# Kernel tuning notes

Hardware: AMD Instinct MI355X
Metric: run time of the kernel (lower is better)

## Reference

```python
import jax, jax.numpy as jnp
import numpy as np

B, M, K, F, H = 4096, 50000, 31, 256, 256
N = K + 1                      # nodes per graph: center + K neighbors
GAMMA = 1.0 / (2.0 * 1.0 ** 2) # rbf_kernel gamma with length_scale = 1.0


def setup_inputs() -> dict:
    key = jax.random.key(0)
    k = jax.random.split(key, 9)
    return {
        "spatial_features": jax.random.normal(k[0], (B, 2), jnp.float32),
        "features": jax.random.normal(k[1], (B, F), jnp.float32),
        "train_spatial": jax.random.normal(k[2], (M, 2), jnp.float32),
        "train_features": jax.random.normal(k[3], (M, F), jnp.float32),
        "train_y": jax.random.normal(k[4], (M, 1), jnp.float32),
        "W0": jax.random.normal(k[5], (F + 2, H), jnp.float32) * (1.0 / np.sqrt(F + 2)),
        "W1": jax.random.normal(k[6], (H, H), jnp.float32) * (1.0 / np.sqrt(H)),
        "W2": jax.random.normal(k[7], (H, H), jnp.float32) * (1.0 / np.sqrt(H)),
        "Wout": jax.random.normal(k[8], (H, 1), jnp.float32) * (1.0 / np.sqrt(H)),
    }


def reference(spatial_features, features, train_spatial, train_features, train_y,
              W0, W1, W2, Wout):
    # --- brute-force kNN over train spatial coords (sklearn kneighbors) ---
    d2 = (jnp.sum(spatial_features ** 2, -1, keepdims=True)
          - 2.0 * spatial_features @ train_spatial.T
          + jnp.sum(train_spatial ** 2, -1)[None, :])                 # [B, M]
    nb = jax.lax.top_k(jax.lax.stop_gradient(-d2), K)[1]              # [B, K] indices

    # --- form_input_graph: node features = [feat ++ y ++ indicator] ---
    feat = jnp.concatenate([features[:, None, :], train_features[nb]], axis=1)    # [B,N,F]
    y = jnp.concatenate([jnp.zeros((B, 1, 1), feat.dtype), train_y[nb]], axis=1)  # [B,N,1]
    ind = jnp.zeros((B, N, 1), feat.dtype).at[:, 0, 0].set(1.0)                   # [B,N,1]
    x = jnp.concatenate([feat, y, ind], axis=-1)                                  # [B,N,F+2]

    # --- dense RBF adjacency: complete graph, self-loops already on diagonal ---
    coords = jnp.concatenate([spatial_features[:, None, :], train_spatial[nb]], axis=1)  # [B,N,2]
    diff = coords[:, :, None, :] - coords[:, None, :, :]
    A = jnp.exp(-GAMMA * jnp.sum(diff * diff, -1))                    # [B,N,N]
    # GCN symmetric normalization D^-1/2 A D^-1/2 (deg > 0 since diag = 1)
    dinv = jax.lax.rsqrt(jnp.sum(A, -1))                              # [B,N]
    Ahat = A * dinv[:, :, None] * dinv[:, None, :]

    h = jax.nn.relu(jnp.einsum('bij,bjh->bih', Ahat, x @ W0))
    h = jax.nn.relu(jnp.einsum('bij,bjh->bih', Ahat, h @ W1))
    h = jax.nn.relu(jnp.einsum('bij,bjh->bih', Ahat, h @ W2))

    # center node -> linear head (bias=False), last_activation='none'
    return h[:, 0] @ Wout                                             # [B, 1]
```

## Files before the change

### kernel.cpp

```cpp
#include <hip/hip_runtime.h>

typedef _Float16 half8 __attribute__((ext_vector_type(8)));
typedef __fp16  fp16x2 __attribute__((ext_vector_type(2)));
typedef float f32x16 __attribute__((ext_vector_type(16)));

#define M_TRAIN 50000
#define NQ 4096
#define KNN 31

#define LO_SCALE 1024.0f
#define LO_INV   9.765625e-4f

__global__ void prep_weights_k(const float* __restrict__ W0,
                               const float* __restrict__ W1,
                               const float* __restrict__ W2,
                               _Float16* __restrict__ W0hi, _Float16* __restrict__ W0lo,
                               _Float16* __restrict__ W1hi, _Float16* __restrict__ W1lo,
                               _Float16* __restrict__ W2hi, _Float16* __restrict__ W2lo) {
    int t = blockIdx.x * 256 + threadIdx.x;
    const int n0 = 17 * 8 * 64, n1 = 16 * 8 * 64, n2 = 16 * 8 * 64;
    if (t >= n0 + n1 + n2) return;
    const float* src; _Float16 *dhi, *dlo; int idx, Kin;
    if (t < n0)           { src = W0; dhi = W0hi; dlo = W0lo; idx = t;           Kin = 258; }
    else if (t < n0 + n1) { src = W1; dhi = W1hi; dlo = W1lo; idx = t - n0;      Kin = 256; }
    else                  { src = W2; dhi = W2hi; dlo = W2lo; idx = t - n0 - n1; Kin = 256; }
    int lane = idx & 63, nt = (idx >> 6) & 7, ks = idx >> 9;
    int col = nt * 32 + (lane & 31);
    int k0  = ks * 16 + (lane >> 5) * 8;
    _Float16 vhi[8], vlo[8];
#pragma unroll
    for (int j = 0; j < 8; j++) {
        int k = k0 + j;
        float w = (k < Kin) ? src[k * 256 + col] : 0.f;
        _Float16 hi = (_Float16)w;
        vhi[j] = hi;
        vlo[j] = (_Float16)((w - (float)hi) * LO_SCALE);
    }
    *reinterpret_cast<uint4*>(dhi + (size_t)idx * 8) = *reinterpret_cast<const uint4*>(vhi);
    *reinterpret_cast<uint4*>(dlo + (size_t)idx * 8) = *reinterpret_cast<const uint4*>(vlo);
}

#define QPB2 4
#define TILE2 2048
#define CAP2 128

__global__ __launch_bounds__(256) void knn_k(const float* __restrict__ qs,
                                             const float* __restrict__ ts,
                                             int* __restrict__ nb) {
    __shared__ __align__(16) float tile[TILE2 * 2];
    __shared__ float  mrg[QPB2][128];
    __shared__ int    ci[QPB2][CAP2];
    __shared__ double chd[QPB2][CAP2];
    __shared__ int    cnt[QPB2];

    const int t = threadIdx.x;
    const int w = t >> 6, lane = t & 63;
    const int q = blockIdx.x * QPB2 + w;

    if (lane == 0) cnt[w] = 0;
    const float qx = qs[q * 2 + 0], qy = qs[q * 2 + 1];
    const float2* tilev = reinterpret_cast<const float2*>(tile);

    float v0 = 3.4e38f, v1 = 3.4e38f;
    for (int base = 0; base < M_TRAIN; base += TILE2) {
        const int n = min(TILE2, M_TRAIN - base);
        __syncthreads();
        for (int i = t; i < n / 2; i += 256)
            reinterpret_cast<float4*>(tile)[i] =
                reinterpret_cast<const float4*>(ts + (size_t)base * 2)[i];
        __syncthreads();
#pragma unroll 4
        for (int p = lane; p < n; p += 64) {
            float2 pt = tilev[p];
            float dx = qx - pt.x, dy = qy - pt.y;
            float d2 = fmaf(dx, dx, dy * dy);
            v1 = fminf(v1, fmaxf(v0, d2));
            v0 = fminf(v0, d2);
        }
    }
    __syncthreads();
    mrg[w][2 * lane]     = v0;
    mrg[w][2 * lane + 1] = v1;
    __syncthreads();

    float xa = mrg[w][lane], xb = mrg[w][64 + lane];
    int lea = 0, leb = 0;
    for (int i = 0; i < 128; i++) {
        float v = mrg[w][i];
        lea += (v <= xa) ? 1 : 0;
        leb += (v <= xb) ? 1 : 0;
    }
    float tc = 3.4e38f;
    if (lea >= 31) tc = xa;
    if (leb >= 31 && xb < tc) tc = xb;
#pragma unroll
    for (int off = 32; off; off >>= 1)
        tc = fminf(tc, __shfl_xor(tc, off));
    const float thr = tc * 1.00001f + 1e-7f;

    for (int base = 0; base < M_TRAIN; base += TILE2) {
        const int n = min(TILE2, M_TRAIN - base);
        __syncthreads();
        for (int i = t; i < n / 2; i += 256)
            reinterpret_cast<float4*>(tile)[i] =
                reinterpret_cast<const float4*>(ts + (size_t)base * 2)[i];
        __syncthreads();
#pragma unroll 4
        for (int p = lane; p < n; p += 64) {
            float2 pt = tilev[p];
            float dx = qx - pt.x, dy = qy - pt.y;
            float d2 = fmaf(dx, dx, dy * dy);
            if (d2 < thr) {
                int pos = atomicAdd(&cnt[w], 1);
                if (pos < CAP2) ci[w][pos] = base + p;
            }
        }
    }
    __syncthreads();

    const int C = min(cnt[w], CAP2);
    for (int c = lane; c < C; c += 64) {
        int idx = ci[w][c];
        double dx = (double)qx - (double)ts[idx * 2];
        double dy = (double)qy - (double)ts[idx * 2 + 1];
        chd[w][c] = dx * dx + dy * dy;
    }
    __syncthreads();
    for (int c = lane; c < C; c += 64) {
        double key = chd[w][c];
        int   idx = ci[w][c];
        int rank = 0;
        for (int o = 0; o < C; o++) {
            double ok = chd[w][o];
            int    oi = ci[w][o];
            rank += ((ok < key) || (ok == key && oi < idx)) ? 1 : 0;
        }
        if (rank < KNN) nb[q * KNN + rank] = idx;
    }
}

#define PX 276
#define PT 36

__device__ inline half8 ld_h8(const _Float16* p) {
    union { half8 h; uint2 u[2]; } r;
    r.u[0] = *reinterpret_cast<const uint2*>(p);
    r.u[1] = *reinterpret_cast<const uint2*>(p + 4);
    return r.h;
}
__device__ inline half8 ld_h8_g(const _Float16* p) {
    union { half8 h; uint4 u; } r;
    r.u = *reinterpret_cast<const uint4*>(p);
    return r.h;
}
__device__ inline f32x16 zero16() {
    f32x16 z;
#pragma unroll
    for (int i = 0; i < 16; i++) z[i] = 0.f;
    return z;
}
__device__ inline unsigned pk_u(float a, float b) {
    union { fp16x2 v; unsigned u; } c;
    c.v = __builtin_amdgcn_cvt_pkrtz(a, b);
    return c.u;
}
__device__ inline float f16lo(unsigned u) {
    union { unsigned u; fp16x2 v; } c; c.u = u; return (float)c.v[0];
}
__device__ inline float f16hi(unsigned u) {
    union { unsigned u; fp16x2 v; } c; c.u = u; return (float)c.v[1];
}
__device__ inline half8 frag_x(const unsigned* w, int ks2, int h) {
    unsigned w0 = w[4 * ks2 + 0], w1 = w[4 * ks2 + 1];
    unsigned w2 = w[4 * ks2 + 2], w3 = w[4 * ks2 + 3];
    unsigned sA = h ? w0 : w2, sB = h ? w1 : w3;
    unsigned rA = __shfl_xor(sA, 32);
    unsigned rB = __shfl_xor(sB, 32);
    unsigned kA = h ? w2 : w0, kB = h ? w3 : w1;
    union { half8 h8; unsigned u[4]; } f;
    f.u[0] = h ? rA : kA;
    f.u[1] = h ? rB : kB;
    f.u[2] = h ? kA : rA;
    f.u[3] = h ? kB : rB;
    return f.h8;
}
#define MFMA(a, b, c) __builtin_amdgcn_mfma_f32_32x32x16_f16((a), (b), (c), 0, 0, 0)

__global__ __launch_bounds__(256, 4) void gcn_k(
    const float* __restrict__ qs, const float* __restrict__ qf,
    const float* __restrict__ ts, const float* __restrict__ tf,
    const float* __restrict__ ty, const float* __restrict__ Wout,
    const int* __restrict__ nb,
    const _Float16* __restrict__ W0hi, const _Float16* __restrict__ W0lo,
    const _Float16* __restrict__ W1hi, const _Float16* __restrict__ W1lo,
    const _Float16* __restrict__ W2hi, const _Float16* __restrict__ W2lo,
    float* __restrict__ out) {
    __shared__ __align__(16) _Float16 Xhi[32 * PX];
    __shared__ __align__(16) _Float16 Xlo[32 * PX];
    __shared__ _Float16 Ahhi[32 * PT];
    __shared__ _Float16 Ahlo[32 * PT];
    __shared__ float coords[64];
    __shared__ float dinv[32];
    __shared__ float yvs[32];
    __shared__ int   idxs[32];

    const int t = threadIdx.x;
    const int w = t >> 6, lane = t & 63;
    const int h = lane >> 5, ln = lane & 31;
    const int q0 = blockIdx.x;

    if (t < 32) {
        int idx = (t == 0) ? -1 : nb[q0 * KNN + (t - 1)];
        idxs[t] = idx;
        const float* c = (t == 0) ? (qs + (size_t)q0 * 2) : (ts + (size_t)idx * 2);
        coords[t * 2 + 0] = c[0];
        coords[t * 2 + 1] = c[1];
        yvs[t] = (t == 0) ? 0.f : ty[idx];
    }
    __syncthreads();

    {
        const float* src0 = (w == 0) ? (qf + (size_t)q0 * 256)
                                     : (tf + (size_t)idxs[w] * 256);
        float4 pv = reinterpret_cast<const float4*>(src0)[lane];
        for (int r = w; r < 32; r += 4) {
            float4 cv = pv;
            int rn = r + 4;
            if (rn < 32)
                pv = reinterpret_cast<const float4*>(tf + (size_t)idxs[rn] * 256)[lane];
            float a4[4] = {cv.x, cv.y, cv.z, cv.w};
            unsigned hw[2], lw[2];
#pragma unroll
            for (int j = 0; j < 2; j++) {
                float x0 = a4[2 * j], x1 = a4[2 * j + 1];
                hw[j] = pk_u(x0, x1);
                lw[j] = pk_u((x0 - f16lo(hw[j])) * LO_SCALE,
                             (x1 - f16hi(hw[j])) * LO_SCALE);
            }
            *reinterpret_cast<uint2*>(&Xhi[r * PX + 4 * lane]) = *reinterpret_cast<uint2*>(hw);
            *reinterpret_cast<uint2*>(&Xlo[r * PX + 4 * lane]) = *reinterpret_cast<uint2*>(lw);
            if (lane == 0) {
                float yv = yvs[r];
                _Float16 thi[16], tlo[16];
#pragma unroll
                for (int j = 0; j < 16; j++) { thi[j] = (_Float16)0.f; tlo[j] = (_Float16)0.f; }
                _Float16 yh = (_Float16)yv;
                thi[0] = yh;
                tlo[0] = (_Float16)((yv - (float)yh) * LO_SCALE);
                thi[1] = (r == 0) ? (_Float16)1.f : (_Float16)0.f;
#pragma unroll
                for (int c = 0; c < 4; c++) {
                    *reinterpret_cast<uint2*>(&Xhi[r * PX + 256 + 4 * c]) = reinterpret_cast<uint2*>(thi)[c];
                    *reinterpret_cast<uint2*>(&Xlo[r * PX + 256 + 4 * c]) = reinterpret_cast<uint2*>(tlo)[c];
                }
            }
        }
    }

    if (t < 64) {
        int i = t >> 1, jh = t & 1;
        float xi = coords[i * 2], yi = coords[i * 2 + 1];
        float part = 0.f;
#pragma unroll
        for (int jj = 0; jj < 16; jj++) {
            int j = jh * 16 + jj;
            float dx = xi - coords[j * 2], dy = yi - coords[j * 2 + 1];
            part += __expf(-0.5f * (dx * dx + dy * dy));
        }
        float asum = part + __shfl_xor(part, 1);
        if (jh == 0) dinv[i] = 1.0f / sqrtf(asum);
    }
    __syncthreads();
    if (t < 64) {
        int i = t >> 1, jh = t & 1;
        float xi = coords[i * 2], yi = coords[i * 2 + 1];
        float di = dinv[i];
        _Float16 ahi[16], alo[16];
#pragma unroll
        for (int jj = 0; jj < 16; jj++) {
            int j = jh * 16 + jj;
            float dx = xi - coords[j * 2], dy = yi - coords[j * 2 + 1];
            float a = __expf(-0.5f * (dx * dx + dy * dy)) * di * dinv[j];
            _Float16 hi = (_Float16)a;
            ahi[jj] = hi;
            alo[jj] = (_Float16)((a - (float)hi) * LO_SCALE);
        }
        _Float16* dh = &Ahhi[i * PT + jh * 16];
        _Float16* dl = &Ahlo[i * PT + jh * 16];
#pragma unroll
        for (int c = 0; c < 4; c++) {
            reinterpret_cast<uint2*>(dh)[c] = reinterpret_cast<uint2*>(ahi)[c];
            reinterpret_cast<uint2*>(dl)[c] = reinterpret_cast<uint2*>(alo)[c];
        }
    }
    __syncthreads();

    const _Float16* Whis[3] = {W0hi, W1hi, W2hi};
    const _Float16* Wlos[3] = {W0lo, W1lo, W2lo};
    for (int layer = 0; layer < 3; layer++) {
        const _Float16* Whi = Whis[layer];
        const _Float16* Wlo = Wlos[layer];
        const int KS = (layer == 0) ? 17 : 16;

        f32x16 acc0 = zero16(), acc1 = zero16();
        f32x16 cor0 = zero16(), cor1 = zero16();
        const int boBase = (2 * w * 64 + lane) * 8;
        const _Float16* Xa = &Xhi[ln * PX + 8 * h];
        const _Float16* Xb = &Xlo[ln * PX + 8 * h];
#pragma unroll 2
        for (int ks = 0; ks < KS; ks++) {
            half8 Ahi_ = ld_h8(Xa + ks * 16);
            half8 Alo_ = ld_h8(Xb + ks * 16);
            int bo = boBase + ks * 4096;
            half8 Bh0 = ld_h8_g(Whi + bo);
            half8 Bh1 = ld_h8_g(Whi + bo + 512);
            half8 Bl0 = ld_h8_g(Wlo + bo);
            half8 Bl1 = ld_h8_g(Wlo + bo + 512);
            acc0 = MFMA(Ahi_, Bh0, acc0);
            cor0 = MFMA(Alo_, Bh0, cor0);
            cor0 = MFMA(Ahi_, Bl0, cor0);
            acc1 = MFMA(Ahi_, Bh1, acc1);
            cor1 = MFMA(Alo_, Bh1, cor1);
            cor1 = MFMA(Ahi_, Bl1, cor1);
        }
        __syncthreads();

        unsigned whi0[8], wlo0[8], whi1[8], wlo1[8];
#pragma unroll
        for (int g = 0; g < 8; g++) {
            float x0 = fmaf(cor0[2 * g],     LO_INV, acc0[2 * g]);
            float x1 = fmaf(cor0[2 * g + 1], LO_INV, acc0[2 * g + 1]);
            unsigned hw = pk_u(x0, x1);
            whi0[g] = hw;
            wlo0[g] = pk_u((x0 - f16lo(hw)) * LO_SCALE, (x1 - f16hi(hw)) * LO_SCALE);
            float y0 = fmaf(cor1[2 * g],     LO_INV, acc1[2 * g]);
            float y1 = fmaf(cor1[2 * g + 1], LO_INV, acc1[2 * g + 1]);
            unsigned hv = pk_u(y0, y1);
            whi1[g] = hv;
            wlo1[g] = pk_u((y0 - f16lo(hv)) * LO_SCALE, (y1 - f16hi(hv)) * LO_SCALE);
        }

        f32x16 p0 = zero16(), p1 = zero16();
        f32x16 pc0 = zero16(), pc1 = zero16();
#pragma unroll
        for (int ks2 = 0; ks2 < 2; ks2++) {
            half8 bAhi = ld_h8(&Ahhi[ln * PT + ks2 * 16 + 8 * h]);
            half8 bAlo = ld_h8(&Ahlo[ln * PT + ks2 * 16 + 8 * h]);
            half8 t0hi = frag_x(whi0, ks2, h);
            half8 t0lo = frag_x(wlo0, ks2, h);
            half8 t1hi = frag_x(whi1, ks2, h);
            half8 t1lo = frag_x(wlo1, ks2, h);
            p0  = MFMA(t0hi, bAhi, p0);
            pc0 = MFMA(t0lo, bAhi, pc0);
            pc0 = MFMA(t0hi, bAlo, pc0);
            p1  = MFMA(t1hi, bAhi, p1);
            pc1 = MFMA(t1lo, bAhi, pc1);
            pc1 = MFMA(t1hi, bAlo, pc1);
        }

#pragma unroll
        for (int a = 0; a < 2; a++) {
            const f32x16& A = a ? p1 : p0;
            const f32x16& C = a ? pc1 : pc0;
#pragma unroll
            for (int c = 0; c < 4; c++) {
                float x0 = fmaf(C[4 * c + 0], LO_INV, A[4 * c + 0]);
                float x1 = fmaf(C[4 * c + 1], LO_INV, A[4 * c + 1]);
                float x2 = fmaf(C[4 * c + 2], LO_INV, A[4 * c + 2]);
                float x3 = fmaf(C[4 * c + 3], LO_INV, A[4 * c + 3]);
                x0 = fmaxf(x0, 0.f); x1 = fmaxf(x1, 0.f);
                x2 = fmaxf(x2, 0.f); x3 = fmaxf(x3, 0.f);
                unsigned hw[2], lw[2];
                hw[0] = pk_u(x0, x1);
                hw[1] = pk_u(x2, x3);
                lw[0] = pk_u((x0 - f16lo(hw[0])) * LO_SCALE, (x1 - f16hi(hw[0])) * LO_SCALE);
                lw[1] = pk_u((x2 - f16lo(hw[1])) * LO_SCALE, (x3 - f16hi(hw[1])) * LO_SCALE);
                int feat = 64 * w + 32 * a + 8 * c + 4 * h;
                *reinterpret_cast<uint2*>(&Xhi[ln * PX + feat]) = *reinterpret_cast<uint2*>(hw);
                *reinterpret_cast<uint2*>(&Xlo[ln * PX + feat]) = *reinterpret_cast<uint2*>(lw);
            }
        }
        __syncthreads();
    }

    if (w == 0) {
        float4 wv = reinterpret_cast<const float4*>(Wout)[lane];
        union { uint2 u; _Float16 f[4]; } hh, hl;
        hh.u = *reinterpret_cast<const uint2*>(&Xhi[4 * lane]);
        hl.u = *reinterpret_cast<const uint2*>(&Xlo[4 * lane]);
        float s = ((float)hh.f[0] + (float)hl.f[0] * LO_INV) * wv.x
                + ((float)hh.f[1] + (float)hl.f[1] * LO_INV) * wv.y
                + ((float)hh.f[2] + (float)hl.f[2] * LO_INV) * wv.z
                + ((float)hh.f[3] + (float)hl.f[3] * LO_INV) * wv.w;
#pragma unroll
        for (int off = 32; off; off >>= 1) s += __shfl_xor(s, off);
        if (lane == 0) out[q0] = s;
    }
}

extern "C" void kernel_launch(void* const* d_in, const int* in_sizes, int n_in,
                              void* d_out, int out_size, void* d_ws, size_t ws_size,
                              hipStream_t stream) {
    const float* qs   = (const float*)d_in[0];
    const float* qf   = (const float*)d_in[1];
    const float* ts   = (const float*)d_in[2];
    const float* tf   = (const float*)d_in[3];
    const float* ty   = (const float*)d_in[4];
    const float* W0   = (const float*)d_in[5];
    const float* W1   = (const float*)d_in[6];
    const float* W2   = (const float*)d_in[7];
    const float* Wout = (const float*)d_in[8];
    float* out = (float*)d_out;

    char* ws = (char*)d_ws;
    int*      nb   = (int*)ws;
    _Float16* W0hi = (_Float16*)(ws + 524288);
    _Float16* W0lo = (_Float16*)(ws + 663552);
    _Float16* W1hi = (_Float16*)(ws + 802816);
    _Float16* W1lo = (_Float16*)(ws + 933888);
    _Float16* W2hi = (_Float16*)(ws + 1064960);
    _Float16* W2lo = (_Float16*)(ws + 1196032);

    hipLaunchKernelGGL(prep_weights_k, dim3(98), dim3(256), 0, stream,
                       W0, W1, W2, W0hi, W0lo, W1hi, W1lo, W2hi, W2lo);
    hipLaunchKernelGGL(knn_k, dim3(NQ / QPB2), dim3(256), 0, stream, qs, ts, nb);
    hipLaunchKernelGGL(gcn_k, dim3(NQ), dim3(256), 0, stream,
                       qs, qf, ts, tf, ty, Wout, nb,
                       W0hi, W0lo, W1hi, W1lo, W2hi, W2lo, out);
}
```

Measured before the change: 327.9 us.

## Process two queries per wave in kNN and split GCN across eight waves

The kNN kernel now gives each wave two queries. Every train point read from the shared tile is reused for two distance computations, and the tile size and queries per block are doubled. The GCN kernel moves to 512-thread blocks, where each wave owns 32 output columns instead of 64. This halves per-wave accumulator registers and MFMA chains, but needs more LDS per block in kNN and may reduce resident blocks.

Measured after the change: 366.6 us. +11.8%, slower.

```diff
diff --git a/kernel.cpp b/kernel.cpp
--- a/kernel.cpp
+++ b/kernel.cpp
@@ -40,8 +40,8 @@
     *reinterpret_cast<uint4*>(dlo + (size_t)idx * 8) = *reinterpret_cast<const uint4*>(vlo);
 }
 
-#define QPB2 4
-#define TILE2 2048
+#define QPB2 8
+#define TILE2 4096
 #define CAP2 128
 
 __global__ __launch_bounds__(256) void knn_k(const float* __restrict__ qs,
@@ -55,13 +55,15 @@
 
     const int t = threadIdx.x;
     const int w = t >> 6, lane = t & 63;
-    const int q = blockIdx.x * QPB2 + w;
-
-    if (lane == 0) cnt[w] = 0;
-    const float qx = qs[q * 2 + 0], qy = qs[q * 2 + 1];
+    const int q0 = blockIdx.x * QPB2;
+    const int qA = q0 + 2 * w, qB = qA + 1;
+
+    if (lane < 2) cnt[2 * w + lane] = 0;
+    const float qxA = qs[qA * 2 + 0], qyA = qs[qA * 2 + 1];
+    const float qxB = qs[qB * 2 + 0], qyB = qs[qB * 2 + 1];
     const float2* tilev = reinterpret_cast<const float2*>(tile);
 
-    float v0 = 3.4e38f, v1 = 3.4e38f;
+    float a0 = 3.4e38f, a1 = 3.4e38f, b0 = 3.4e38f, b1 = 3.4e38f;
     for (int base = 0; base < M_TRAIN; base += TILE2) {
         const int n = min(TILE2, M_TRAIN - base);
         __syncthreads();
@@ -72,31 +74,41 @@
 #pragma unroll 4
         for (int p = lane; p < n; p += 64) {
             float2 pt = tilev[p];
-            float dx = qx - pt.x, dy = qy - pt.y;
-            float d2 = fmaf(dx, dx, dy * dy);
-            v1 = fminf(v1, fmaxf(v0, d2));
-            v0 = fminf(v0, d2);
-        }
-    }
-    __syncthreads();
-    mrg[w][2 * lane]     = v0;
-    mrg[w][2 * lane + 1] = v1;
-    __syncthreads();
-
-    float xa = mrg[w][lane], xb = mrg[w][64 + lane];
-    int lea = 0, leb = 0;
-    for (int i = 0; i < 128; i++) {
-        float v = mrg[w][i];
-        lea += (v <= xa) ? 1 : 0;
-        leb += (v <= xb) ? 1 : 0;
-    }
-    float tc = 3.4e38f;
-    if (lea >= 31) tc = xa;
-    if (leb >= 31 && xb < tc) tc = xb;
-#pragma unroll
-    for (int off = 32; off; off >>= 1)
-        tc = fminf(tc, __shfl_xor(tc, off));
-    const float thr = tc * 1.00001f + 1e-7f;
+            float dxA = qxA - pt.x, dyA = qyA - pt.y;
+            float dA = fmaf(dxA, dxA, dyA * dyA);
+            a1 = fminf(a1, fmaxf(a0, dA));
+            a0 = fminf(a0, dA);
+            float dxB = qxB - pt.x, dyB = qyB - pt.y;
+            float dB = fmaf(dxB, dxB, dyB * dyB);
+            b1 = fminf(b1, fmaxf(b0, dB));
+            b0 = fminf(b0, dB);
+        }
+    }
+    __syncthreads();
+    mrg[2 * w + 0][2 * lane] = a0; mrg[2 * w + 0][2 * lane + 1] = a1;
+    mrg[2 * w + 1][2 * lane] = b0; mrg[2 * w + 1][2 * lane + 1] = b1;
+    __syncthreads();
+
+    float thrq[2];
+#pragma unroll
+    for (int qq = 0; qq < 2; qq++) {
+        const int qi = 2 * w + qq;
+        float xa = mrg[qi][lane], xb = mrg[qi][64 + lane];
+        int lea = 0, leb = 0;
+        for (int i = 0; i < 128; i++) {
+            float v = mrg[qi][i];
+            lea += (v <= xa) ? 1 : 0;
+            leb += (v <= xb) ? 1 : 0;
+        }
+        float tc = 3.4e38f;
+        if (lea >= 31) tc = xa;
+        if (leb >= 31 && xb < tc) tc = xb;
+#pragma unroll
+        for (int off = 32; off; off >>= 1)
+            tc = fminf(tc, __shfl_xor(tc, off));
+        thrq[qq] = tc * 1.00001f + 1e-7f;
+    }
+    const float thrA = thrq[0], thrB = thrq[1];
 
     for (int base = 0; base < M_TRAIN; base += TILE2) {
         const int n = min(TILE2, M_TRAIN - base);
@@ -108,34 +120,46 @@
 #pragma unroll 4
         for (int p = lane; p < n; p += 64) {
             float2 pt = tilev[p];
-            float dx = qx - pt.x, dy = qy - pt.y;
-            float d2 = fmaf(dx, dx, dy * dy);
-            if (d2 < thr) {
-                int pos = atomicAdd(&cnt[w], 1);
-                if (pos < CAP2) ci[w][pos] = base + p;
+            float dxA = qxA - pt.x, dyA = qyA - pt.y;
+            float dA = fmaf(dxA, dxA, dyA * dyA);
+            if (dA < thrA) {
+                int pos = atomicAdd(&cnt[2 * w + 0], 1);
+                if (pos < CAP2) ci[2 * w + 0][pos] = base + p;
             }
-        }
-    }
-    __syncthreads();
-
-    const int C = min(cnt[w], CAP2);
-    for (int c = lane; c < C; c += 64) {
-        int idx = ci[w][c];
-        double dx = (double)qx - (double)ts[idx * 2];
-        double dy = (double)qy - (double)ts[idx * 2 + 1];
-        chd[w][c] = dx * dx + dy * dy;
-    }
-    __syncthreads();
-    for (int c = lane; c < C; c += 64) {
-        double key = chd[w][c];
-        int   idx = ci[w][c];
-        int rank = 0;
-        for (int o = 0; o < C; o++) {
-            double ok = chd[w][o];
-            int    oi = ci[w][o];
-            rank += ((ok < key) || (ok == key && oi < idx)) ? 1 : 0;
-        }
-        if (rank < KNN) nb[q * KNN + rank] = idx;
+            float dxB = qxB - pt.x, dyB = qyB - pt.y;
+            float dB = fmaf(dxB, dxB, dyB * dyB);
+            if (dB < thrB) {
+                int pos = atomicAdd(&cnt[2 * w + 1], 1);
+                if (pos < CAP2) ci[2 * w + 1][pos] = base + p;
+            }
+        }
+    }
+    __syncthreads();
+
+#pragma unroll
+    for (int qq = 0; qq < 2; qq++) {
+        const int qi = 2 * w + qq;
+        const int q  = q0 + qi;
+        const float qx = qq ? qxB : qxA, qy = qq ? qyB : qyA;
+        const int C = min(cnt[qi], CAP2);
+        for (int c = lane; c < C; c += 64) {
+            int idx = ci[qi][c];
+            double dx = (double)qx - (double)ts[idx * 2];
+            double dy = (double)qy - (double)ts[idx * 2 + 1];
+            chd[qi][c] = dx * dx + dy * dy;
+        }
+        __syncthreads();
+        for (int c = lane; c < C; c += 64) {
+            double key = chd[qi][c];
+            int   idx = ci[qi][c];
+            int rank = 0;
+            for (int o = 0; o < C; o++) {
+                double ok = chd[qi][o];
+                int    oi = ci[qi][o];
+                rank += ((ok < key) || (ok == key && oi < idx)) ? 1 : 0;
+            }
+            if (rank < KNN) nb[q * KNN + rank] = idx;
+        }
     }
 }
 
@@ -186,7 +210,7 @@
 }
 #define MFMA(a, b, c) __builtin_amdgcn_mfma_f32_32x32x16_f16((a), (b), (c), 0, 0, 0)
 
-__global__ __launch_bounds__(256, 4) void gcn_k(
+__global__ __launch_bounds__(512, 8) void gcn_k(
     const float* __restrict__ qs, const float* __restrict__ qf,
     const float* __restrict__ ts, const float* __restrict__ tf,
     const float* __restrict__ ty, const float* __restrict__ Wout,
@@ -223,9 +247,9 @@
         const float* src0 = (w == 0) ? (qf + (size_t)q0 * 256)
                                      : (tf + (size_t)idxs[w] * 256);
         float4 pv = reinterpret_cast<const float4*>(src0)[lane];
-        for (int r = w; r < 32; r += 4) {
+        for (int r = w; r < 32; r += 8) {
             float4 cv = pv;
-            int rn = r + 4;
+            int rn = r + 8;
             if (rn < 32)
                 pv = reinterpret_cast<const float4*>(tf + (size_t)idxs[rn] * 256)[lane];
             float a4[4] = {cv.x, cv.y, cv.z, cv.w};
@@ -302,9 +326,9 @@
         const _Float16* Wlo = Wlos[layer];
         const int KS = (layer == 0) ? 17 : 16;
 
-        f32x16 acc0 = zero16(), acc1 = zero16();
-        f32x16 cor0 = zero16(), cor1 = zero16();
-        const int boBase = (2 * w * 64 + lane) * 8;
+        f32x16 acc = zero16();
+        f32x16 cor = zero16();
+        const int boBase = (w * 64 + lane) * 8;
         const _Float16* Xa = &Xhi[ln * PX + 8 * h];
         const _Float16* Xb = &Xlo[ln * PX + 8 * h];
 #pragma unroll 2
@@ -312,73 +336,52 @@
             half8 Ahi_ = ld_h8(Xa + ks * 16);
             half8 Alo_ = ld_h8(Xb + ks * 16);
             int bo = boBase + ks * 4096;
-            half8 Bh0 = ld_h8_g(Whi + bo);
-            half8 Bh1 = ld_h8_g(Whi + bo + 512);
-            half8 Bl0 = ld_h8_g(Wlo + bo);
-            half8 Bl1 = ld_h8_g(Wlo + bo + 512);
-            acc0 = MFMA(Ahi_, Bh0, acc0);
-            cor0 = MFMA(Alo_, Bh0, cor0);
-            cor0 = MFMA(Ahi_, Bl0, cor0);
-            acc1 = MFMA(Ahi_, Bh1, acc1);
-            cor1 = MFMA(Alo_, Bh1, cor1);
-            cor1 = MFMA(Ahi_, Bl1, cor1);
-        }
-        __syncthreads();
-
-        unsigned whi0[8], wlo0[8], whi1[8], wlo1[8];
+            half8 Bh = ld_h8_g(Whi + bo);
+            half8 Bl = ld_h8_g(Wlo + bo);
+            acc = MFMA(Ahi_, Bh, acc);
+            cor = MFMA(Alo_, Bh, cor);
+            cor = MFMA(Ahi_, Bl, cor);
+        }
+        __syncthreads();
+
+        unsigned whi[8], wlo[8];
 #pragma unroll
         for (int g = 0; g < 8; g++) {
-            float x0 = fmaf(cor0[2 * g],     LO_INV, acc0[2 * g]);
-            float x1 = fmaf(cor0[2 * g + 1], LO_INV, acc0[2 * g + 1]);
+            float x0 = fmaf(cor[2 * g],     LO_INV, acc[2 * g]);
+            float x1 = fmaf(cor[2 * g + 1], LO_INV, acc[2 * g + 1]);
             unsigned hw = pk_u(x0, x1);
-            whi0[g] = hw;
-            wlo0[g] = pk_u((x0 - f16lo(hw)) * LO_SCALE, (x1 - f16hi(hw)) * LO_SCALE);
-            float y0 = fmaf(cor1[2 * g],     LO_INV, acc1[2 * g]);
-            float y1 = fmaf(cor1[2 * g + 1], LO_INV, acc1[2 * g + 1]);
-            unsigned hv = pk_u(y0, y1);
-            whi1[g] = hv;
-            wlo1[g] = pk_u((y0 - f16lo(hv)) * LO_SCALE, (y1 - f16hi(hv)) * LO_SCALE);
-        }
-
-        f32x16 p0 = zero16(), p1 = zero16();
-        f32x16 pc0 = zero16(), pc1 = zero16();
+            whi[g] = hw;
+            wlo[g] = pk_u((x0 - f16lo(hw)) * LO_SCALE, (x1 - f16hi(hw)) * LO_SCALE);
+        }
+
+        f32x16 p = zero16(), pc = zero16();
 #pragma unroll
         for (int ks2 = 0; ks2 < 2; ks2++) {
             half8 bAhi = ld_h8(&Ahhi[ln * PT + ks2 * 16 + 8 * h]);
             half8 bAlo = ld_h8(&Ahlo[ln * PT + ks2 * 16 + 8 * h]);
-            half8 t0hi = frag_x(whi0, ks2, h);
-            half8 t0lo = frag_x(wlo0, ks2, h);
-            half8 t1hi = frag_x(whi1, ks2, h);
-            half8 t1lo = frag_x(wlo1, ks2, h);
-            p0  = MFMA(t0hi, bAhi, p0);
-            pc0 = MFMA(t0lo, bAhi, pc0);
-            pc0 = MFMA(t0hi, bAlo, pc0);
-            p1  = MFMA(t1hi, bAhi, p1);
-            pc1 = MFMA(t1lo, bAhi, pc1);
-            pc1 = MFMA(t1hi, bAlo, pc1);
-        }
-
-#pragma unroll
-        for (int a = 0; a < 2; a++) {
-            const f32x16& A = a ? p1 : p0;
-            const f32x16& C = a ? pc1 : pc0;
-#pragma unroll
-            for (int c = 0; c < 4; c++) {
-                float x0 = fmaf(C[4 * c + 0], LO_INV, A[4 * c + 0]);
-                float x1 = fmaf(C[4 * c + 1], LO_INV, A[4 * c + 1]);
-                float x2 = fmaf(C[4 * c + 2], LO_INV, A[4 * c + 2]);
-                float x3 = fmaf(C[4 * c + 3], LO_INV, A[4 * c + 3]);
-                x0 = fmaxf(x0, 0.f); x1 = fmaxf(x1, 0.f);
-                x2 = fmaxf(x2, 0.f); x3 = fmaxf(x3, 0.f);
-                unsigned hw[2], lw[2];
-                hw[0] = pk_u(x0, x1);
-                hw[1] = pk_u(x2, x3);
-                lw[0] = pk_u((x0 - f16lo(hw[0])) * LO_SCALE, (x1 - f16hi(hw[0])) * LO_SCALE);
-                lw[1] = pk_u((x2 - f16lo(hw[1])) * LO_SCALE, (x3 - f16hi(hw[1])) * LO_SCALE);
-                int feat = 64 * w + 32 * a + 8 * c + 4 * h;
-                *reinterpret_cast<uint2*>(&Xhi[ln * PX + feat]) = *reinterpret_cast<uint2*>(hw);
-                *reinterpret_cast<uint2*>(&Xlo[ln * PX + feat]) = *reinterpret_cast<uint2*>(lw);
-            }
+            half8 thi = frag_x(whi, ks2, h);
+            half8 tlo = frag_x(wlo, ks2, h);
+            p  = MFMA(thi, bAhi, p);
+            pc = MFMA(tlo, bAhi, pc);
+            pc = MFMA(thi, bAlo, pc);
+        }
+
+#pragma unroll
+        for (int c = 0; c < 4; c++) {
+            float x0 = fmaf(pc[4 * c + 0], LO_INV, p[4 * c + 0]);
+            float x1 = fmaf(pc[4 * c + 1], LO_INV, p[4 * c + 1]);
+            float x2 = fmaf(pc[4 * c + 2], LO_INV, p[4 * c + 2]);
+            float x3 = fmaf(pc[4 * c + 3], LO_INV, p[4 * c + 3]);
+            x0 = fmaxf(x0, 0.f); x1 = fmaxf(x1, 0.f);
+            x2 = fmaxf(x2, 0.f); x3 = fmaxf(x3, 0.f);
+            unsigned hw[2], lw[2];
+            hw[0] = pk_u(x0, x1);
+            hw[1] = pk_u(x2, x3);
+            lw[0] = pk_u((x0 - f16lo(hw[0])) * LO_SCALE, (x1 - f16hi(hw[0])) * LO_SCALE);
+            lw[1] = pk_u((x2 - f16lo(hw[1])) * LO_SCALE, (x3 - f16hi(hw[1])) * LO_SCALE);
+            int feat = 32 * w + 8 * c + 4 * h;
+            *reinterpret_cast<uint2*>(&Xhi[ln * PX + feat]) = *reinterpret_cast<uint2*>(hw);
+            *reinterpret_cast<uint2*>(&Xlo[ln * PX + feat]) = *reinterpret_cast<uint2*>(lw);
         }
         __syncthreads();
     }
@@ -424,7 +427,7 @@
     hipLaunchKernelGGL(prep_weights_k, dim3(98), dim3(256), 0, stream,
                        W0, W1, W2, W0hi, W0lo, W1hi, W1lo, W2hi, W2lo);
     hipLaunchKernelGGL(knn_k, dim3(NQ / QPB2), dim3(256), 0, stream, qs, ts, nb);
-    hipLaunchKernelGGL(gcn_k, dim3(NQ), dim3(256), 0, stream,
+    hipLaunchKernelGGL(gcn_k, dim3(NQ), dim3(512), 0, stream,
                        qs, qf, ts, tf, ty, Wout, nb,
                        W0hi, W0lo, W1hi, W1lo, W2hi, W2lo, out);
 }
```

## Process two query graphs per block to share weight fragment loads

Applied to the files above, without the earlier changes.

Each gcn block now handles two query graphs with 512 threads instead of one graph with 256 threads. Each of the eight waves covers 32 output features and reuses the same W hi/lo fragment for both graphs' 32-row tiles. This halves global weight traffic per graph and doubles the per-block LDS footprint. The risk is lower occupancy from the larger LDS and thread count, and a launch bound of 512x4 that may pressure registers.

Result: faster. 315.9 us, median of 2 (-3.7%).

```diff
diff --git a/kernel.cpp b/kernel.cpp
--- a/kernel.cpp
+++ b/kernel.cpp
@@ -186,7 +186,7 @@
 }
 #define MFMA(a, b, c) __builtin_amdgcn_mfma_f32_32x32x16_f16((a), (b), (c), 0, 0, 0)
 
-__global__ __launch_bounds__(256, 4) void gcn_k(
+__global__ __launch_bounds__(512, 4) void gcn_k(
     const float* __restrict__ qs, const float* __restrict__ qf,
     const float* __restrict__ ts, const float* __restrict__ tf,
     const float* __restrict__ ty, const float* __restrict__ Wout,
@@ -195,39 +195,43 @@
     const _Float16* __restrict__ W1hi, const _Float16* __restrict__ W1lo,
     const _Float16* __restrict__ W2hi, const _Float16* __restrict__ W2lo,
     float* __restrict__ out) {
-    __shared__ __align__(16) _Float16 Xhi[32 * PX];
-    __shared__ __align__(16) _Float16 Xlo[32 * PX];
-    __shared__ _Float16 Ahhi[32 * PT];
-    __shared__ _Float16 Ahlo[32 * PT];
-    __shared__ float coords[64];
-    __shared__ float dinv[32];
-    __shared__ float yvs[32];
-    __shared__ int   idxs[32];
+    __shared__ __align__(16) _Float16 Xhi[64 * PX];
+    __shared__ __align__(16) _Float16 Xlo[64 * PX];
+    __shared__ _Float16 Ahhi[2 * 32 * PT];
+    __shared__ _Float16 Ahlo[2 * 32 * PT];
+    __shared__ float coords[128];
+    __shared__ float dinv[64];
+    __shared__ float yvs[64];
+    __shared__ int   idxs[64];
 
     const int t = threadIdx.x;
     const int w = t >> 6, lane = t & 63;
     const int h = lane >> 5, ln = lane & 31;
-    const int q0 = blockIdx.x;
-
-    if (t < 32) {
-        int idx = (t == 0) ? -1 : nb[q0 * KNN + (t - 1)];
+    const int g2 = blockIdx.x * 2;
+
+    if (t < 64) {
+        int g = t >> 5, n = t & 31;
+        int idx = (n == 0) ? -1 : nb[(g2 + g) * KNN + (n - 1)];
         idxs[t] = idx;
-        const float* c = (t == 0) ? (qs + (size_t)q0 * 2) : (ts + (size_t)idx * 2);
+        const float* c = (n == 0) ? (qs + (size_t)(g2 + g) * 2) : (ts + (size_t)idx * 2);
         coords[t * 2 + 0] = c[0];
         coords[t * 2 + 1] = c[1];
-        yvs[t] = (t == 0) ? 0.f : ty[idx];
+        yvs[t] = (n == 0) ? 0.f : ty[idx];
     }
     __syncthreads();
 
     {
-        const float* src0 = (w == 0) ? (qf + (size_t)q0 * 256)
-                                     : (tf + (size_t)idxs[w] * 256);
-        float4 pv = reinterpret_cast<const float4*>(src0)[lane];
-        for (int r = w; r < 32; r += 4) {
+        const float* s0 = ((w & 31) == 0) ? (qf + (size_t)(g2 + (w >> 5)) * 256)
+                                          : (tf + (size_t)idxs[w] * 256);
+        float4 pv = reinterpret_cast<const float4*>(s0)[lane];
+        for (int r = w; r < 64; r += 8) {
             float4 cv = pv;
-            int rn = r + 4;
-            if (rn < 32)
-                pv = reinterpret_cast<const float4*>(tf + (size_t)idxs[rn] * 256)[lane];
+            int rn = r + 8;
+            if (rn < 64) {
+                const float* sn = ((rn & 31) == 0) ? (qf + (size_t)(g2 + (rn >> 5)) * 256)
+                                                   : (tf + (size_t)idxs[rn] * 256);
+                pv = reinterpret_cast<const float4*>(sn)[lane];
+            }
             float a4[4] = {cv.x, cv.y, cv.z, cv.w};
             unsigned hw[2], lw[2];
 #pragma unroll
@@ -247,7 +251,7 @@
                 _Float16 yh = (_Float16)yv;
                 thi[0] = yh;
                 tlo[0] = (_Float16)((yv - (float)yh) * LO_SCALE);
-                thi[1] = (r == 0) ? (_Float16)1.f : (_Float16)0.f;
+                thi[1] = ((r & 31) == 0) ? (_Float16)1.f : (_Float16)0.f;
 #pragma unroll
                 for (int c = 0; c < 4; c++) {
                     *reinterpret_cast<uint2*>(&Xhi[r * PX + 256 + 4 * c]) = reinterpret_cast<uint2*>(thi)[c];
@@ -257,36 +261,38 @@
         }
     }
 
-    if (t < 64) {
-        int i = t >> 1, jh = t & 1;
-        float xi = coords[i * 2], yi = coords[i * 2 + 1];
+    if (t < 128) {
+        int g = t >> 6, i = (t >> 1) & 31, jh = t & 1;
+        int ni = g * 32 + i;
+        float xi = coords[ni * 2], yi = coords[ni * 2 + 1];
         float part = 0.f;
 #pragma unroll
         for (int jj = 0; jj < 16; jj++) {
-            int j = jh * 16 + jj;
-            float dx = xi - coords[j * 2], dy = yi - coords[j * 2 + 1];
+            int nj = g * 32 + jh * 16 + jj;
+            float dx = xi - coords[nj * 2], dy = yi - coords[nj * 2 + 1];
             part += __expf(-0.5f * (dx * dx + dy * dy));
         }
         float asum = part + __shfl_xor(part, 1);
-        if (jh == 0) dinv[i] = 1.0f / sqrtf(asum);
-    }
-    __syncthreads();
-    if (t < 64) {
-        int i = t >> 1, jh = t & 1;
-        float xi = coords[i * 2], yi = coords[i * 2 + 1];
-        float di = dinv[i];
+        if (jh == 0) dinv[ni] = 1.0f / sqrtf(asum);
+    }
+    __syncthreads();
+    if (t < 128) {
+        int g = t >> 6, i = (t >> 1) & 31, jh = t & 1;
+        int ni = g * 32 + i;
+        float xi = coords[ni * 2], yi = coords[ni * 2 + 1];
+        float di = dinv[ni];
         _Float16 ahi[16], alo[16];
 #pragma unroll
         for (int jj = 0; jj < 16; jj++) {
-            int j = jh * 16 + jj;
-            float dx = xi - coords[j * 2], dy = yi - coords[j * 2 + 1];
-            float a = __expf(-0.5f * (dx * dx + dy * dy)) * di * dinv[j];
+            int nj = g * 32 + jh * 16 + jj;
+            float dx = xi - coords[nj * 2], dy = yi - coords[nj * 2 + 1];
+            float a = __expf(-0.5f * (dx * dx + dy * dy)) * di * dinv[nj];
             _Float16 hi = (_Float16)a;
             ahi[jj] = hi;
             alo[jj] = (_Float16)((a - (float)hi) * LO_SCALE);
         }
-        _Float16* dh = &Ahhi[i * PT + jh * 16];
-        _Float16* dl = &Ahlo[i * PT + jh * 16];
+        _Float16* dh = &Ahhi[ni * PT + jh * 16];
+        _Float16* dl = &Ahlo[ni * PT + jh * 16];
 #pragma unroll
         for (int c = 0; c < 4; c++) {
             reinterpret_cast<uint2*>(dh)[c] = reinterpret_cast<uint2*>(ahi)[c];
@@ -302,26 +308,28 @@
         const _Float16* Wlo = Wlos[layer];
         const int KS = (layer == 0) ? 17 : 16;
 
-        f32x16 acc0 = zero16(), acc1 = zero16();
-        f32x16 cor0 = zero16(), cor1 = zero16();
-        const int boBase = (2 * w * 64 + lane) * 8;
-        const _Float16* Xa = &Xhi[ln * PX + 8 * h];
-        const _Float16* Xb = &Xlo[ln * PX + 8 * h];
+        f32x16 acc0 = zero16(), cor0 = zero16();
+        f32x16 acc1 = zero16(), cor1 = zero16();
+        const int boBase = (w * 64 + lane) * 8;
+        const _Float16* Xa0 = &Xhi[ln * PX + 8 * h];
+        const _Float16* Xb0 = &Xlo[ln * PX + 8 * h];
+        const _Float16* Xa1 = &Xhi[(32 + ln) * PX + 8 * h];
+        const _Float16* Xb1 = &Xlo[(32 + ln) * PX + 8 * h];
 #pragma unroll 2
         for (int ks = 0; ks < KS; ks++) {
-            half8 Ahi_ = ld_h8(Xa + ks * 16);
-            half8 Alo_ = ld_h8(Xb + ks * 16);
             int bo = boBase + ks * 4096;
-            half8 Bh0 = ld_h8_g(Whi + bo);
-            half8 Bh1 = ld_h8_g(Whi + bo + 512);
-            half8 Bl0 = ld_h8_g(Wlo + bo);
-            half8 Bl1 = ld_h8_g(Wlo + bo + 512);
-            acc0 = MFMA(Ahi_, Bh0, acc0);
-            cor0 = MFMA(Alo_, Bh0, cor0);
-            cor0 = MFMA(Ahi_, Bl0, cor0);
-            acc1 = MFMA(Ahi_, Bh1, acc1);
-            cor1 = MFMA(Alo_, Bh1, cor1);
-            cor1 = MFMA(Ahi_, Bl1, cor1);
+            half8 Bh = ld_h8_g(Whi + bo);
+            half8 Bl = ld_h8_g(Wlo + bo);
+            half8 A0h = ld_h8(Xa0 + ks * 16);
+            half8 A0l = ld_h8(Xb0 + ks * 16);
+            half8 A1h = ld_h8(Xa1 + ks * 16);
+            half8 A1l = ld_h8(Xb1 + ks * 16);
+            acc0 = MFMA(A0h, Bh, acc0);
+            cor0 = MFMA(A0l, Bh, cor0);
+            cor0 = MFMA(A0h, Bl, cor0);
+            acc1 = MFMA(A1h, Bh, acc1);
+            cor1 = MFMA(A1l, Bh, cor1);
+            cor1 = MFMA(A1h, Bl, cor1);
         }
         __syncthreads();
 
@@ -340,34 +348,37 @@
             wlo1[g] = pk_u((y0 - f16lo(hv)) * LO_SCALE, (y1 - f16hi(hv)) * LO_SCALE);
         }
 
-        f32x16 p0 = zero16(), p1 = zero16();
-        f32x16 pc0 = zero16(), pc1 = zero16();
+        f32x16 p0 = zero16(), pc0 = zero16();
+        f32x16 p1 = zero16(), pc1 = zero16();
 #pragma unroll
         for (int ks2 = 0; ks2 < 2; ks2++) {
-            half8 bAhi = ld_h8(&Ahhi[ln * PT + ks2 * 16 + 8 * h]);
-            half8 bAlo = ld_h8(&Ahlo[ln * PT + ks2 * 16 + 8 * h]);
+            half8 bA0h = ld_h8(&Ahhi[ln * PT + ks2 * 16 + 8 * h]);
+            half8 bA0l = ld_h8(&Ahlo[ln * PT + ks2 * 16 + 8 * h]);
+            half8 bA1h = ld_h8(&Ahhi[(32 + ln) * PT + ks2 * 16 + 8 * h]);
+            half8 bA1l = ld_h8(&Ahlo[(32 + ln) * PT + ks2 * 16 + 8 * h]);
             half8 t0hi = frag_x(whi0, ks2, h);
             half8 t0lo = frag_x(wlo0, ks2, h);
             half8 t1hi = frag_x(whi1, ks2, h);
             half8 t1lo = frag_x(wlo1, ks2, h);
-            p0  = MFMA(t0hi, bAhi, p0);
-            pc0 = MFMA(t0lo, bAhi, pc0);
-            pc0 = MFMA(t0hi, bAlo, pc0);
-            p1  = MFMA(t1hi, bAhi, p1);
-            pc1 = MFMA(t1lo, bAhi, pc1);
-            pc1 = MFMA(t1hi, bAlo, pc1);
-        }
-
-#pragma unroll
-        for (int a = 0; a < 2; a++) {
-            const f32x16& A = a ? p1 : p0;
-            const f32x16& C = a ? pc1 : pc0;
+            p0  = MFMA(t0hi, bA0h, p0);
+            pc0 = MFMA(t0lo, bA0h, pc0);
+            pc0 = MFMA(t0hi, bA0l, pc0);
+            p1  = MFMA(t1hi, bA1h, p1);
+            pc1 = MFMA(t1lo, bA1h, pc1);
+            pc1 = MFMA(t1hi, bA1l, pc1);
+        }
+
+#pragma unroll
+        for (int g = 0; g < 2; g++) {
+            const f32x16& P = g ? p1 : p0;
+            const f32x16& C = g ? pc1 : pc0;
+            int row = g * 32 + ln;
 #pragma unroll
             for (int c = 0; c < 4; c++) {
-                float x0 = fmaf(C[4 * c + 0], LO_INV, A[4 * c + 0]);
-                float x1 = fmaf(C[4 * c + 1], LO_INV, A[4 * c + 1]);
-                float x2 = fmaf(C[4 * c + 2], LO_INV, A[4 * c + 2]);
-                float x3 = fmaf(C[4 * c + 3], LO_INV, A[4 * c + 3]);
+                float x0 = fmaf(C[4 * c + 0], LO_INV, P[4 * c + 0]);
+                float x1 = fmaf(C[4 * c + 1], LO_INV, P[4 * c + 1]);
+                float x2 = fmaf(C[4 * c + 2], LO_INV, P[4 * c + 2]);
+                float x3 = fmaf(C[4 * c + 3], LO_INV, P[4 * c + 3]);
                 x0 = fmaxf(x0, 0.f); x1 = fmaxf(x1, 0.f);
                 x2 = fmaxf(x2, 0.f); x3 = fmaxf(x3, 0.f);
                 unsigned hw[2], lw[2];
@@ -375,26 +386,26 @@
                 hw[1] = pk_u(x2, x3);
                 lw[0] = pk_u((x0 - f16lo(hw[0])) * LO_SCALE, (x1 - f16hi(hw[0])) * LO_SCALE);
                 lw[1] = pk_u((x2 - f16lo(hw[1])) * LO_SCALE, (x3 - f16hi(hw[1])) * LO_SCALE);
-                int feat = 64 * w + 32 * a + 8 * c + 4 * h;
-                *reinterpret_cast<uint2*>(&Xhi[ln * PX + feat]) = *reinterpret_cast<uint2*>(hw);
-                *reinterpret_cast<uint2*>(&Xlo[ln * PX + feat]) = *reinterpret_cast<uint2*>(lw);
+                int feat = 32 * w + 8 * c + 4 * h;
+                *reinterpret_cast<uint2*>(&Xhi[row * PX + feat]) = *reinterpret_cast<uint2*>(hw);
+                *reinterpret_cast<uint2*>(&Xlo[row * PX + feat]) = *reinterpret_cast<uint2*>(lw);
             }
         }
         __syncthreads();
     }
 
-    if (w == 0) {
+    if (w < 2) {
         float4 wv = reinterpret_cast<const float4*>(Wout)[lane];
         union { uint2 u; _Float16 f[4]; } hh, hl;
-        hh.u = *reinterpret_cast<const uint2*>(&Xhi[4 * lane]);
-        hl.u = *reinterpret_cast<const uint2*>(&Xlo[4 * lane]);
+        hh.u = *reinterpret_cast<const uint2*>(&Xhi[(w * 32) * PX + 4 * lane]);
+        hl.u = *reinterpret_cast<const uint2*>(&Xlo[(w * 32) * PX + 4 * lane]);
         float s = ((float)hh.f[0] + (float)hl.f[0] * LO_INV) * wv.x
                 + ((float)hh.f[1] + (float)hl.f[1] * LO_INV) * wv.y
                 + ((float)hh.f[2] + (float)hl.f[2] * LO_INV) * wv.z
                 + ((float)hh.f[3] + (float)hl.f[3] * LO_INV) * wv.w;
 #pragma unroll
         for (int off = 32; off; off >>= 1) s += __shfl_xor(s, off);
-        if (lane == 0) out[q0] = s;
+        if (lane == 0) out[g2 + w] = s;
     }
 }
 
@@ -424,7 +435,7 @@
     hipLaunchKernelGGL(prep_weights_k, dim3(98), dim3(256), 0, stream,
                        W0, W1, W2, W0hi, W0lo, W1hi, W1lo, W2hi, W2lo);
     hipLaunchKernelGGL(knn_k, dim3(NQ / QPB2), dim3(256), 0, stream, qs, ts, nb);
-    hipLaunchKernelGGL(gcn_k, dim3(NQ), dim3(256), 0, stream,
+    hipLaunchKernelGGL(gcn_k, dim3(NQ / 2), dim3(512), 0, stream,
                        qs, qf, ts, tf, ty, Wout, nb,
                        W0hi, W0lo, W1hi, W1lo, W2hi, W2lo, out);
 }
```
